# Kernel tuning notes

Measured on AMD Instinct MI355X. Metric: run time of the kernel, lower is better.

The kernel has to match this reference:

```python
import jax, jax.numpy as jnp
import numpy as np

N_ORB = 1024    # Monte-Carlo orbits
NTIMES = 1024   # observation epochs
N_FZ = 24       # zodi flux grid points (uniform in log10)
N_KEZ = 6       # exozodi multipliers (sorted, searchsorted lookup)
N_TINT = 64     # integration times
N_ALPHA = 512   # separations (uniform in log10)


def setup_inputs() -> dict:
    key = jax.random.key(0)
    k1, k2, k3, k4 = jax.random.split(key, 4)
    fZs = jnp.logspace(-10.0, -7.0, N_FZ).astype(jnp.float32)
    alphas = jnp.logspace(-2.0, 1.0, N_ALPHA).astype(jnp.float32)
    kEZs = jnp.array([0.5, 1.0, 2.0, 5.0, 10.0, 20.0], dtype=jnp.float32)
    # grid already in the module's internal (n_fZ, n_kEZ, n_tint, n_alpha) layout
    grid = 25.0 + jax.random.normal(k1, (N_FZ, N_KEZ, N_TINT, N_ALPHA), dtype=jnp.float32)
    # alpha slightly exceeds [alphas[0], alphas[-1]] so geom_mask is exercised
    alpha = (10.0 ** jax.random.uniform(k2, (N_ORB, NTIMES), minval=-2.2, maxval=1.1)).astype(jnp.float32)
    dMag = (25.0 + jax.random.normal(k3, (N_ORB, NTIMES))).astype(jnp.float32)
    fZ_vals = (10.0 ** jax.random.uniform(k4, (NTIMES,), minval=-10.0, maxval=-7.0)).astype(jnp.float32)
    kEZ_val = jnp.float32(1.5)
    return dict(alpha=alpha, dMag=dMag, fZ_vals=fZ_vals, kEZ_val=kEZ_val,
                grid=grid, fZs=fZs, kEZs=kEZs, alphas=alphas)


def reference(alpha, dMag, fZ_vals, kEZ_val, grid, fZs, kEZs, alphas):
    """Faithful vectorized translation of dMag0Grid._pdet_alpha_dMag.

    alpha, dMag: (n_orb, ntimes); fZ_vals: (ntimes,); kEZ_val: scalar;
    grid: (n_fZ, n_kEZ, n_tint, n_alpha). Returns pdet (ntimes, n_tint).
    """
    n_fZ = fZs.shape[0]
    n_alpha = alphas.shape[0]
    log_fZs = jnp.log10(fZs)
    inv_log_fZ_step = 1.0 / (log_fZs[1] - log_fZs[0])
    log_alphas = jnp.log10(alphas)
    inv_log_alpha_step = 1.0 / (log_alphas[1] - log_alphas[0])

    geom_mask = (alpha >= alphas[0]) & (alpha <= alphas[-1])          # (n_orb, ntimes)

    fZ_ind = (jnp.log10(fZ_vals) - log_fZs[0]) * inv_log_fZ_step
    fZ0 = jnp.clip(jnp.floor(fZ_ind).astype(jnp.int32) + 1, 0, n_fZ - 2)  # (ntimes,)

    a_ind = (jnp.log10(alpha) - log_alphas[0]) * inv_log_alpha_step
    a0 = jnp.clip(a_ind.astype(jnp.int32), 0, n_alpha - 1)               # (n_orb, ntimes)
    dalpha = (a_ind - a0).astype(grid.dtype)

    kEZ_ind = jnp.searchsorted(kEZs, kEZ_val, side='right') - 1

    # lax.dynamic_slice clamps the start so the width-2 window fits:
    s = jnp.minimum(a0, n_alpha - 2)                                     # (n_orb, ntimes)

    g = jnp.take(grid, kEZ_ind, axis=1)                                  # (n_fZ, n_tint, n_alpha)
    g_f = g[fZ0]                                                          # (ntimes, n_tint, n_alpha)
    sT = s.T                                                              # (ntimes, n_orb)
    g0 = jnp.take_along_axis(g_f, sT[:, None, :], axis=2)                 # (ntimes, n_tint, n_orb)
    g1 = jnp.take_along_axis(g_f, (sT + 1)[:, None, :], axis=2)
    res = g0 + dalpha.T[:, None, :] * (g1 - g0)                           # (ntimes, n_tint, n_orb)

    dim = jnp.transpose(res, (2, 0, 1))                                   # (n_orb, ntimes, n_tint)
    det_mask = geom_mask[..., None] & jnp.signbit(dMag[..., None] - dim)
    pdet = det_mask.astype(jnp.float32).mean(axis=0)                      # (ntimes, n_tint)
    return pdet
```

## Files before the change

### kernel.cpp

```cpp
#include <hip/hip_runtime.h>
#include <math.h>

#define N_ORB   1024
#define NTIMES  1024
#define N_FZ    24
#define N_KEZ   6
#define N_TINT  64
#define N_ALPHA 512

#define SL_STRIDE 33

#define GT_BYTES (N_FZ * N_ALPHA * N_TINT * 4)

__global__ __launch_bounds__(256) void stage_inputs(
    const float* __restrict__ grid, const float* __restrict__ kEZs,
    const float* __restrict__ kEZ_val_p, const float* __restrict__ alpha,
    const float* __restrict__ dMag, const float* __restrict__ alphas,
    float* __restrict__ gT, float2* __restrict__ Pc)
{
    __shared__ float lds[64 * 65];

    int b = blockIdx.x;
    if (b < 192) {
        float kv = kEZ_val_p[0];
        int cnt = 0;
#pragma unroll
        for (int i = 0; i < N_KEZ; ++i) cnt += (kEZs[i] <= kv) ? 1 : 0;
        int kez = cnt - 1;
        kez = kez < 0 ? 0 : (kez > N_KEZ - 1 ? N_KEZ - 1 : kez);

        int fz = b >> 3, sc = b & 7;
        int w = threadIdx.x >> 6, lane = threadIdx.x & 63;
        const float* gsrc = grid + ((size_t)fz * N_KEZ + kez) * N_TINT * N_ALPHA;

#pragma unroll
        for (int r = 0; r < 16; ++r) {
            int tint = w * 16 + r;
            lds[tint * 65 + lane] = gsrc[(size_t)tint * N_ALPHA + sc * 64 + lane];
        }
        __syncthreads();
#pragma unroll
        for (int r = 0; r < 16; ++r) {
            int sl = w * 16 + r;
            gT[((size_t)fz * N_ALPHA + sc * 64 + sl) * N_TINT + lane] = lds[lane * 65 + sl];
        }
    } else {
        float* ut = lds;
        float* dt = lds + 1056;

        int u = b - 192;
        int t0 = (u & 31) * 32, o0 = (u >> 5) * 32;
        int row = threadIdx.x >> 5, col = threadIdx.x & 31;

        float al0 = alphas[0], al1 = alphas[N_ALPHA - 1];
        float la0 = log10f(al0);
        float inv_step = 1.0f / (log10f(alphas[1]) - la0);

#pragma unroll
        for (int r = 0; r < 4; ++r) {
            int ol = r * 8 + row;
            size_t idx = (size_t)(o0 + ol) * NTIMES + t0 + col;
            float a = alpha[idx];
            float d = dMag[idx];
            float a_ind = (log10f(a) - la0) * inv_step;
            int a0i = (int)a_ind;
            a0i = a0i < 0 ? 0 : (a0i > N_ALPHA - 1 ? N_ALPHA - 1 : a0i);
            float dal = a_ind - (float)a0i;
            int s = a0i > N_ALPHA - 2 ? N_ALPHA - 2 : a0i;
            bool geom = (a >= al0) && (a <= al1);
            float uv = (float)s + dal;
            uv = fminf(fmaxf(uv, 0.0f), 510.999f);
            if (!geom) uv = 0.0f;
            ut[ol * 33 + col] = uv;
            dt[ol * 33 + col] = geom ? d : __builtin_inff();
        }
        __syncthreads();
#pragma unroll
        for (int r = 0; r < 4; ++r) {
            int tl = r * 8 + row;
            float2 v;
            v.x = ut[col * 33 + tl];
            v.y = dt[col * 33 + tl];
            Pc[(size_t)(t0 + tl) * N_ORB + o0 + col] = v;
        }
    }
}

__global__ __launch_bounds__(256) void pdet_main(
    const float* __restrict__ fZ_vals, const float* __restrict__ fZs,
    const float* __restrict__ gT, const float2* __restrict__ Pc,
    float* __restrict__ out)
{
    __shared__ float  sl[N_ALPHA * SL_STRIDE];
    __shared__ float2 PcL[N_ORB];
    __shared__ int    red[128];

    int t = blockIdx.x >> 1;
    int h = blockIdx.x & 1;
    int tid = threadIdx.x;

    float lf0 = log10f(fZs[0]);
    float inv_f = 1.0f / (log10f(fZs[1]) - lf0);
    float fi = (log10f(fZ_vals[t]) - lf0) * inv_f;
    int f0 = (int)floorf(fi) + 1;
    f0 = f0 < 0 ? 0 : (f0 > N_FZ - 2 ? N_FZ - 2 : f0);

    const float*  gB = gT + (size_t)f0 * N_ALPHA * N_TINT + h * 32;
    const float2* Pt = Pc + (size_t)t * N_ORB;

    {
        int srow = tid >> 3;
        int jj   = tid & 7;
#pragma unroll
        for (int it = 0; it < 16; ++it) {
            int s = it * 32 + srow;
            float4 g = *reinterpret_cast<const float4*>(gB + (size_t)s * N_TINT + jj * 4);
            float* dst = &sl[s * SL_STRIDE + jj * 4];
            dst[0] = g.x; dst[1] = g.y; dst[2] = g.z; dst[3] = g.w;
        }
    }
#pragma unroll
    for (int it = 0; it < 4; ++it)
        PcL[it * 256 + tid] = Pt[it * 256 + tid];
    __syncthreads();

    int w = tid >> 6, lane = tid & 63;
    int half = lane >> 5;
    int j    = lane & 31;

    int obase = w * 256 + half;
    int cnt = 0;

#pragma unroll 8
    for (int k = 0; k < 128; ++k) {
        float2 p = PcL[obase + 2 * k];
        float u = p.x, dm = p.y;
        int su = (int)u;
        const float* r0 = &sl[su * SL_STRIDE + j];
        float g0 = r0[0];
        float g1 = r0[SL_STRIDE];
        cnt += dm < fmaf(u - (float)su, g1 - g0, g0);
    }

    cnt += __shfl_xor(cnt, 32);
    if (lane < 32) red[w * 32 + lane] = cnt;
    __syncthreads();
    if (tid < 32) {
        int tot = red[tid] + red[32 + tid] + red[64 + tid] + red[96 + tid];
        out[(size_t)t * N_TINT + h * 32 + tid] = (float)tot * (1.0f / 1024.0f);
    }
}

extern "C" void kernel_launch(void* const* d_in, const int* in_sizes, int n_in,
                              void* d_out, int out_size, void* d_ws, size_t ws_size,
                              hipStream_t stream) {
    const float* alpha   = (const float*)d_in[0];
    const float* dMag    = (const float*)d_in[1];
    const float* fZ_vals = (const float*)d_in[2];
    const float* kEZ_val = (const float*)d_in[3];
    const float* grid    = (const float*)d_in[4];
    const float* fZs     = (const float*)d_in[5];
    const float* kEZs    = (const float*)d_in[6];
    const float* alphas  = (const float*)d_in[7];
    float*  out = (float*)d_out;

    float*  gT = (float*)d_ws;
    float2* Pc = (float2*)((char*)d_ws + GT_BYTES);

    stage_inputs<<<dim3(192 + 1024), 256, 0, stream>>>(
        grid, kEZs, kEZ_val, alpha, dMag, alphas, gT, Pc);
    pdet_main<<<dim3(NTIMES * 2), 256, 0, stream>>>(fZ_vals, fZs, gT, Pc, out);
}
```

Before: 111.4 us.

## Compute two tint columns per lane and read orbit data directly from global

```diff
diff --git a/kernel.cpp b/kernel.cpp
--- a/kernel.cpp
+++ b/kernel.cpp
@@ -8,7 +8,7 @@
 #define N_TINT  64
 #define N_ALPHA 512
 
-#define SL_STRIDE 33
+#define SL_STRIDE 34
 
 #define GT_BYTES (N_FZ * N_ALPHA * N_TINT * 4)
 
@@ -91,9 +91,8 @@
     const float* __restrict__ gT, const float2* __restrict__ Pc,
     float* __restrict__ out)
 {
-    __shared__ float  sl[N_ALPHA * SL_STRIDE];
-    __shared__ float2 PcL[N_ORB];
-    __shared__ int    red[128];
+    __shared__ float sl[N_ALPHA * SL_STRIDE];
+    __shared__ int   red[4 * 32];
 
     int t = blockIdx.x >> 1;
     int h = blockIdx.x & 1;
@@ -108,42 +107,46 @@
     const float*  gB = gT + (size_t)f0 * N_ALPHA * N_TINT + h * 32;
     const float2* Pt = Pc + (size_t)t * N_ORB;
 
-    {
-        int srow = tid >> 3;
-        int jj   = tid & 7;
 #pragma unroll
-        for (int it = 0; it < 16; ++it) {
-            int s = it * 32 + srow;
-            float4 g = *reinterpret_cast<const float4*>(gB + (size_t)s * N_TINT + jj * 4);
-            float* dst = &sl[s * SL_STRIDE + jj * 4];
-            dst[0] = g.x; dst[1] = g.y; dst[2] = g.z; dst[3] = g.w;
-        }
+    for (int it = 0; it < 16; ++it) {
+        int idx = it * 256 + tid;
+        int s = idx >> 3, jj = idx & 7;
+        float4 g = *reinterpret_cast<const float4*>(gB + (size_t)s * N_TINT + jj * 4);
+        float* dst = &sl[s * SL_STRIDE + jj * 4];
+        dst[0] = g.x; dst[1] = g.y; dst[2] = g.z; dst[3] = g.w;
     }
-#pragma unroll
-    for (int it = 0; it < 4; ++it)
-        PcL[it * 256 + tid] = Pt[it * 256 + tid];
     __syncthreads();
 
     int w = tid >> 6, lane = tid & 63;
-    int half = lane >> 5;
-    int j    = lane & 31;
+    int o  = lane >> 4;
+    int tp = lane & 15;
+    int tb = tp * 2;
 
-    int obase = w * 256 + half;
-    int cnt = 0;
+    const float2* Pw = Pt + w * 256 + o;
+
+    int c0 = 0, c1 = 0;
 
 #pragma unroll 8
-    for (int k = 0; k < 128; ++k) {
-        float2 p = PcL[obase + 2 * k];
+    for (int k = 0; k < 64; ++k) {
+        float2 p = Pw[k * 4];
         float u = p.x, dm = p.y;
         int su = (int)u;
-        const float* r0 = &sl[su * SL_STRIDE + j];
-        float g0 = r0[0];
-        float g1 = r0[SL_STRIDE];
-        cnt += dm < fmaf(u - (float)su, g1 - g0, g0);
+        float fr = u - (float)su;
+        const float* r = &sl[su * SL_STRIDE + tb];
+        float g00 = r[0];
+        float g01 = r[1];
+        float g10 = r[SL_STRIDE];
+        float g11 = r[SL_STRIDE + 1];
+        c0 += dm < fmaf(fr, g10 - g00, g00);
+        c1 += dm < fmaf(fr, g11 - g01, g01);
     }
 
-    cnt += __shfl_xor(cnt, 32);
-    if (lane < 32) red[w * 32 + lane] = cnt;
+    c0 += __shfl_xor(c0, 16); c0 += __shfl_xor(c0, 32);
+    c1 += __shfl_xor(c1, 16); c1 += __shfl_xor(c1, 32);
+    if (lane < 16) {
+        red[w * 32 + tp * 2]     = c0;
+        red[w * 32 + tp * 2 + 1] = c1;
+    }
     __syncthreads();
     if (tid < 32) {
         int tot = red[tid] + red[32 + tid] + red[64 + tid] + red[96 + tid];
```

Measured after the change: 112.3 us. About the same (+0.8%).
